# Kernel optimization log

Hardware: AMD Instinct MI355X
Metric: run time of the kernel (lower is better)

The kernel has to match this reference:

```python
import jax, jax.numpy as jnp
import numpy as np

LRU_DIM = 256
HIDDEN = 256
H = 64
N = LRU_DIM // H  # 4 (even, per assert)
R_MIN, R_MAX, MAX_PHASE = 0.9, 0.999, 6.28
BSZ, T = 8, 4096


def _rotate_half(x):
    # interleaved pairs: [x0,x1,x2,x3,...] -> [-x1,x0,-x3,x2,...]
    r = jnp.stack([-x[..., 1::2], x[..., 0::2]], axis=-1)
    return r.reshape(x.shape)


def _mix_sequence(gamma, thetas, Us):
    # gamma: scalar, thetas: (N/2,), Us: (T,B,N) -> (T,B,N)
    Tlen = Us.shape[0]
    gammas = jnp.broadcast_to(gamma, (Tlen,))
    ths = jnp.broadcast_to(thetas, (Tlen,) + thetas.shape)

    def binf(a, b):
        gi, ti, xi = a
        gj, tj, xj = b
        theta = jnp.repeat(tj, 2, axis=-1)            # (T, N): [t0,t0,t1,t1,...]
        sin = jnp.sin(theta)[..., None, :]            # (T,1,N)
        cos = jnp.cos(theta)[..., None, :]
        acc = gj[..., None, None] * (cos * xi + sin * _rotate_half(xi)) + xj
        return (gi * gj, ti + tj, acc)

    _, _, res = jax.lax.associative_scan(binf, (gammas, ths, Us), axis=0)
    return res


def setup_inputs() -> dict:
    key = jax.random.key(0)
    ks = jax.random.split(key, 7)
    scale = 1.0 / np.sqrt(HIDDEN + LRU_DIM)
    u = jax.random.normal(ks[0], (BSZ, HIDDEN, T), dtype=jnp.float32)
    thetas_log = jnp.log(jax.random.uniform(ks[1], (H, N // 2), minval=0.01, maxval=1.0) * MAX_PHASE).astype(jnp.float32)
    P_param = (jax.random.normal(ks[2], (H, N, N), dtype=jnp.float32) / np.sqrt(LRU_DIM + N)).astype(jnp.float32)
    B_param = (jax.random.normal(ks[3], (H, N, HIDDEN), dtype=jnp.float32) * scale).astype(jnp.float32)
    C = (jax.random.normal(ks[4], (HIDDEN, LRU_DIM), dtype=jnp.float32) * scale).astype(jnp.float32)
    D = jax.random.normal(ks[5], (HIDDEN,), dtype=jnp.float32)
    u1 = jax.random.uniform(ks[6], (H,))
    gamma_log = (np.log(-np.log(R_MAX)) + u1 * (np.log(-np.log(R_MIN)) - np.log(-np.log(R_MAX)))).astype(jnp.float32)
    return {"u": u, "thetas_log": thetas_log, "P_param": P_param,
            "B_param": B_param, "C": C, "D": D, "gamma_log": gamma_log}


def reference(u, thetas_log, P_param, B_param, C, D, gamma_log):
    Bsz, hidden, Tlen = u.shape
    ut = jnp.transpose(u, (0, 2, 1))                       # (B,T,Dh)
    gamma = jnp.exp(-jnp.exp(gamma_log))                   # (H,)
    trace_per_head = jnp.sum(B_param * B_param, axis=(1, 2))  # tr(B B^T) per head
    norm = jnp.sqrt((1.0 - gamma ** 2) / trace_per_head)
    B_norm = norm[:, None, None] * B_param                 # (H,N,Dh)
    skew = P_param - jnp.swapaxes(P_param, 1, 2)
    P = jax.vmap(jax.scipy.linalg.expm)(skew)              # (H,N,N), orthogonal
    Us = jnp.einsum('HnD,BTD->HTBn', B_norm, ut)           # (H,T,B,N)
    Us = jnp.einsum('HNn,HTBn->HTBN', P, Us)               # == einsum with P^T as in torch
    thetas = jnp.exp(thetas_log)                           # (H,N/2)
    y = jax.vmap(_mix_sequence)(gamma, thetas, Us)         # (H,T,B,N)
    y = jnp.einsum('HNn,HTBN->HTBn', P, y)
    y = jnp.transpose(y, (2, 1, 0, 3)).reshape(Bsz, Tlen, -1)  # (B,T,lru_dim)
    y = jnp.einsum('Dn,BTn->BTD', C, y) + D * ut
    return jnp.transpose(y, (0, 2, 1))                     # (B,Dh,T)
```

## Files before the change

kernel.cpp:

```cpp
#include <hip/hip_runtime.h>
#include <math.h>


typedef __attribute__((ext_vector_type(8))) short short8;
typedef __attribute__((ext_vector_type(4))) float f32x4;

#define TLEN 4096
#define LCH 32
#define NCH 128
#define BSZ 8
#define LDW 132
#define LDK 264

constexpr int MB_OFF   = 0;
constexpr int CB_OFF   = 32768;
constexpr int AP_OFF   = 65536;
constexpr int ALP_OFF  = AP_OFF + (LCH + 1) * 256;
constexpr int TOT_OFF  = ALP_OFF + (NCH + 1) * 256;
constexpr int ZST_OFF  = TOT_OFF + NCH * BSZ * 256;

__device__ __forceinline__ float bfbits2f(unsigned int bits16) {
  union { unsigned int u; float f; } v; v.u = bits16 << 16; return v.f;
}
__device__ __forceinline__ unsigned int f2bfbits(float f) {
  union { float f; unsigned int u; } v; v.f = f;
  return (v.u + 0x7fffu + ((v.u >> 16) & 1u)) >> 16;
}
__device__ __forceinline__ unsigned int pack2(float x, float y) {
  return f2bfbits(x) | (f2bfbits(y) << 16);
}

__global__ __launch_bounds__(256) void k0_setup(
    const float* __restrict__ thetas_log, const float* __restrict__ P_param,
    const float* __restrict__ B_param, const float* __restrict__ C,
    const float* __restrict__ gamma_log, float* __restrict__ ws) {
  const int h = blockIdx.x;
  const int tid = threadIdx.x;
  __shared__ float red[4];
  __shared__ float Psh[16];
  __shared__ float nrmsh;

  {
    float4 v = *(const float4*)(B_param + (size_t)h * 1024 + tid * 4);
    float s = v.x * v.x + v.y * v.y + v.z * v.z + v.w * v.w;
#pragma unroll
    for (int off = 32; off > 0; off >>= 1) s += __shfl_down(s, off);
    if ((tid & 63) == 0) red[tid >> 6] = s;
  }
  __syncthreads();

  if (tid == 0) {
    double A[4][4], E[4][4], Tm[4][4];
    for (int i = 0; i < 4; ++i)
      for (int j = 0; j < 4; ++j)
        A[i][j] = (double)P_param[h * 16 + i * 4 + j] - (double)P_param[h * 16 + j * 4 + i];
    double fro = 0.0;
    for (int i = 0; i < 4; ++i) for (int j = 0; j < 4; ++j) fro += A[i][j] * A[i][j];
    fro = sqrt(fro);
    int s = 0;
    while (fro > 0.25 && s < 30) { fro *= 0.5; ++s; }
    double scl = 1.0;
    for (int q2 = 0; q2 < s; ++q2) scl *= 0.5;
    for (int i = 0; i < 4; ++i) for (int j = 0; j < 4; ++j) A[i][j] *= scl;
    for (int i = 0; i < 4; ++i)
      for (int j = 0; j < 4; ++j) { E[i][j] = (i == j) ? 1.0 : 0.0; Tm[i][j] = E[i][j]; }
    for (int k = 1; k <= 16; ++k) {
      double Tn[4][4];
      for (int i = 0; i < 4; ++i)
        for (int j = 0; j < 4; ++j) {
          double acc = 0.0;
          for (int m = 0; m < 4; ++m) acc += Tm[i][m] * A[m][j];
          Tn[i][j] = acc / (double)k;
        }
      for (int i = 0; i < 4; ++i)
        for (int j = 0; j < 4; ++j) { Tm[i][j] = Tn[i][j]; E[i][j] += Tn[i][j]; }
    }
    for (int q2 = 0; q2 < s; ++q2) {
      double E2[4][4];
      for (int i = 0; i < 4; ++i)
        for (int j = 0; j < 4; ++j) {
          double acc = 0.0;
          for (int m = 0; m < 4; ++m) acc += E[i][m] * E[m][j];
          E2[i][j] = acc;
        }
      for (int i = 0; i < 4; ++i) for (int j = 0; j < 4; ++j) E[i][j] = E2[i][j];
    }
    for (int i = 0; i < 4; ++i)
      for (int j = 0; j < 4; ++j) Psh[i * 4 + j] = (float)E[i][j];
  } else if (tid == 64 || tid == 65) {
    const int p = h * 2 + (tid - 64);
    double th = exp((double)thetas_log[p]);
    double g = exp(-exp((double)gamma_log[h]));
    double ar = g * cos(th), ai = g * sin(th);
    float2* Apw = (float2*)(ws + AP_OFF);
    double xr = 1.0, xi = 0.0;
    Apw[p] = make_float2(1.f, 0.f);
    for (int j = 1; j <= LCH; ++j) {
      double nr = xr * ar - xi * ai, ni = xr * ai + xi * ar;
      xr = nr; xi = ni;
      Apw[j * 128 + p] = make_float2((float)xr, (float)xi);
    }
  } else if (tid == 128) {
    double g = exp(-exp((double)gamma_log[h]));
    double tr = (double)red[0] + red[1] + red[2] + red[3];
    nrmsh = (float)sqrt((1.0 - g * g) / tr);
  }
  __syncthreads();

  unsigned short* Mbf = (unsigned short*)(ws + MB_OFF);
  unsigned int*   Cbd = (unsigned int*)(ws + CB_OFF);
  {
    float b0 = B_param[(h * 4 + 0) * 256 + tid];
    float b1 = B_param[(h * 4 + 1) * 256 + tid];
    float b2 = B_param[(h * 4 + 2) * 256 + tid];
    float b3 = B_param[(h * 4 + 3) * 256 + tid];
    float nrm = nrmsh;
#pragma unroll
    for (int N = 0; N < 4; ++N) {
      float acc = Psh[N * 4 + 0] * b0 + Psh[N * 4 + 1] * b1 +
                  Psh[N * 4 + 2] * b2 + Psh[N * 4 + 3] * b3;
      Mbf[(h * 4 + N) * 256 + tid] = (unsigned short)f2bfbits(nrm * acc);
    }
  }
  {
    float4 cv = *(const float4*)(C + (size_t)tid * 256 + h * 4);
    float o[4];
#pragma unroll
    for (int N = 0; N < 4; ++N)
      o[N] = cv.x * Psh[N * 4 + 0] + cv.y * Psh[N * 4 + 1] +
             cv.z * Psh[N * 4 + 2] + cv.w * Psh[N * 4 + 3];
    Cbd[(tid * 256 + h * 4) >> 1]       = pack2(o[0], o[1]);
    Cbd[((tid * 256 + h * 4) >> 1) + 1] = pack2(o[2], o[3]);
  }
}

__global__ __launch_bounds__(256, 4) void k1_mfma(
    const float* __restrict__ u, float* __restrict__ ws) {
  __shared__ __align__(16) unsigned short us[LCH * LDK];
  __shared__ __align__(16) unsigned int   wd[LCH * LDW];

  const int c = blockIdx.x, b = blockIdx.y;
  const int t0 = c * LCH;
  const int tid = threadIdx.x;
  const int L = tid & 63;
  const int w = __builtin_amdgcn_readfirstlane(tid >> 6);
  const int qh = L >> 4, l15 = L & 15;

  {
    unsigned int* usd = (unsigned int*)us;
    const int dp = tid >> 3;
    const int t4 = (tid & 7) * 4;
    f32x4 va[4], vb[4];
#pragma unroll
    for (int i = 0; i < 4; ++i) {
      int j = dp + 32 * i;
      va[i] = *(const f32x4*)(u + (size_t)(b * 256 + 2 * j) * TLEN + t0 + t4);
      vb[i] = *(const f32x4*)(u + (size_t)(b * 256 + 2 * j + 1) * TLEN + t0 + t4);
    }
#pragma unroll
    for (int i = 0; i < 4; ++i) {
      int j = dp + 32 * i;
#pragma unroll
      for (int dt = 0; dt < 4; ++dt)
        usd[(t4 + dt) * LDW + j] = pack2(va[i][dt], vb[i][dt]);
    }
  }
  __syncthreads();

  f32x4 acc[4][2];
#pragma unroll
  for (int rt = 0; rt < 4; ++rt)
#pragma unroll
    for (int tt = 0; tt < 2; ++tt) acc[rt][tt] = (f32x4){0.f, 0.f, 0.f, 0.f};
  {
    const unsigned short* Mbf = (const unsigned short*)(ws + MB_OFF);
#pragma unroll
    for (int ks = 0; ks < 8; ++ks) {
      short8 af[4], bf[2];
#pragma unroll
      for (int rt = 0; rt < 4; ++rt)
        af[rt] = *(const short8*)(Mbf + (size_t)(w * 64 + rt * 16 + l15) * 256 + ks * 32 + qh * 8);
#pragma unroll
      for (int tt = 0; tt < 2; ++tt)
        bf[tt] = *(const short8*)(us + (tt * 16 + l15) * LDK + ks * 32 + qh * 8);
#pragma unroll
      for (int rt = 0; rt < 4; ++rt)
#pragma unroll
        for (int tt = 0; tt < 2; ++tt)
          acc[rt][tt] = __builtin_amdgcn_mfma_f32_16x16x32_bf16(af[rt], bf[tt], acc[rt][tt], 0, 0, 0);
    }
  }

#pragma unroll
  for (int rt = 0; rt < 4; ++rt) {
    int pbase = w * 32 + rt * 8 + qh * 2;
#pragma unroll
    for (int tt = 0; tt < 2; ++tt) {
      int t = tt * 16 + l15;
      f32x4 a4 = acc[rt][tt];
      wd[t * LDW + pbase]     = pack2(a4[0], a4[1]);
      wd[t * LDW + pbase + 1] = pack2(a4[2], a4[3]);
    }
  }
  __syncthreads();

  if (tid < 128) {
    const int p = tid;
    const float2* Apw = (const float2*)(ws + AP_OFF);
    unsigned int* Zg = (unsigned int*)(ws + ZST_OFF) + (size_t)(c * BSZ + b) * 4096;
    float2 a = Apw[128 + p];
    float zr = 0.f, zi = 0.f;
#pragma unroll
    for (int t = 0; t < LCH; ++t) {
      unsigned int wv = wd[t * LDW + p];
      float wr = bfbits2f(wv & 0xffffu), wi = bfbits2f(wv >> 16);
      float nr = fmaf(a.x, zr, fmaf(-a.y, zi, wr));
      float ni = fmaf(a.x, zi, fmaf(a.y, zr, wi));
      zr = nr; zi = ni;
      Zg[t * 128 + p] = pack2(zr, zi);
    }
    ((float2*)(ws + TOT_OFF))[(c * BSZ + b) * 128 + p] = make_float2(zr, zi);
  }
}

__global__ __launch_bounds__(128) void k2_carry(float* __restrict__ ws) {
  const int b = blockIdx.x;
  const int p = threadIdx.x;
  const float2* Apw = (const float2*)(ws + AP_OFF);
  float2* Tot = (float2*)(ws + TOT_OFF);
  const float2 aL = Apw[LCH * 128 + p];
  float cr = 0.f, ci = 0.f;
  for (int c0 = 0; c0 < NCH; c0 += 16) {
    float2 tv[16];
#pragma unroll
    for (int k = 0; k < 16; ++k)
      tv[k] = Tot[(size_t)((c0 + k) * BSZ + b) * 128 + p];
#pragma unroll
    for (int k = 0; k < 16; ++k) {
      Tot[(size_t)((c0 + k) * BSZ + b) * 128 + p] = make_float2(cr, ci);
      float nr = fmaf(aL.x, cr, fmaf(-aL.y, ci, tv[k].x));
      float ni = fmaf(aL.x, ci, fmaf(aL.y, cr, tv[k].y));
      cr = nr; ci = ni;
    }
  }
}

__global__ __launch_bounds__(256, 4) void k3_mfma(
    const float* __restrict__ u, const float* __restrict__ Dv,
    const float* __restrict__ ws, float* __restrict__ out) {
  __shared__ __align__(16) unsigned char smem[LCH * LDK * 2];
  unsigned int* wd = (unsigned int*)smem;

  const int c = blockIdx.x, b = blockIdx.y;
  const int t0 = c * LCH;
  const int tid = threadIdx.x;
  const int L = tid & 63;
  const int w = __builtin_amdgcn_readfirstlane(tid >> 6);
  const int qh = L >> 4, l15 = L & 15;

  {
    const int p = tid & 127;
    const float2 cv = ((const float2*)(ws + TOT_OFF))[(size_t)(c * BSZ + b) * 128 + p];
    const float2* Apw = (const float2*)(ws + AP_OFF);
    const unsigned int* Zg = (const unsigned int*)(ws + ZST_OFF) + (size_t)(c * BSZ + b) * 4096;
    unsigned int zv[16];
#pragma unroll
    for (int jj = 0; jj < 16; ++jj)
      zv[jj] = Zg[tid + 256 * jj];
#pragma unroll
    for (int jj = 0; jj < 16; ++jj) {
      int t = (tid + 256 * jj) >> 7;
      float2 ap = Apw[(t + 1) * 128 + p];
      float sr = fmaf(ap.x, cv.x, fmaf(-ap.y, cv.y, bfbits2f(zv[jj] & 0xffffu)));
      float si = fmaf(ap.x, cv.y, fmaf(ap.y, cv.x, bfbits2f(zv[jj] >> 16)));
      wd[t * LDW + p] = pack2(sr, si);
    }
  }
  __syncthreads();

  f32x4 acc[4][2];
#pragma unroll
  for (int rt = 0; rt < 4; ++rt)
#pragma unroll
    for (int tt = 0; tt < 2; ++tt) acc[rt][tt] = (f32x4){0.f, 0.f, 0.f, 0.f};
  {
    const unsigned short* Cbf = (const unsigned short*)(ws + CB_OFF);
    const unsigned short* zs  = (const unsigned short*)smem;
#pragma unroll
    for (int ks = 0; ks < 8; ++ks) {
      short8 af[4], bf[2];
#pragma unroll
      for (int rt = 0; rt < 4; ++rt)
        af[rt] = *(const short8*)(Cbf + (size_t)(w * 64 + rt * 16 + l15) * 256 + ks * 32 + qh * 8);
#pragma unroll
      for (int tt = 0; tt < 2; ++tt)
        bf[tt] = *(const short8*)(zs + (tt * 16 + l15) * LDK + ks * 32 + qh * 8);
#pragma unroll
      for (int rt = 0; rt < 4; ++rt)
#pragma unroll
        for (int tt = 0; tt < 2; ++tt)
          acc[rt][tt] = __builtin_amdgcn_mfma_f32_16x16x32_bf16(af[rt], bf[tt], acc[rt][tt], 0, 0, 0);
    }
  }

  float dv[4][4];
#pragma unroll
  for (int rt = 0; rt < 4; ++rt)
#pragma unroll
    for (int q = 0; q < 4; ++q) dv[rt][q] = Dv[w * 64 + rt * 16 + qh * 4 + q];
#pragma unroll
  for (int rt = 0; rt < 4; ++rt) {
    int Dbase = w * 64 + rt * 16 + qh * 4;
#pragma unroll
    for (int tt = 0; tt < 2; ++tt) {
      int t = tt * 16 + l15;
      f32x4 a4 = acc[rt][tt];
      size_t obase = (size_t)(b * 256 + Dbase) * TLEN + t0 + t;
      float uv[4];
#pragma unroll
      for (int q = 0; q < 4; ++q)
        uv[q] = u[obase + (size_t)q * TLEN];
#pragma unroll
      for (int q = 0; q < 4; ++q)
        out[obase + (size_t)q * TLEN] = a4[q] + dv[rt][q] * uv[q];
    }
  }
}

extern "C" void kernel_launch(void* const* d_in, const int* in_sizes, int n_in,
                              void* d_out, int out_size, void* d_ws, size_t ws_size,
                              hipStream_t stream) {
  const float* u          = (const float*)d_in[0];
  const float* thetas_log = (const float*)d_in[1];
  const float* P_param    = (const float*)d_in[2];
  const float* B_param    = (const float*)d_in[3];
  const float* C          = (const float*)d_in[4];
  const float* Dvec       = (const float*)d_in[5];
  const float* gamma_log  = (const float*)d_in[6];
  float* out = (float*)d_out;
  float* ws  = (float*)d_ws;

  hipLaunchKernelGGL(k0_setup, dim3(64), dim3(256), 0, stream,
                     thetas_log, P_param, B_param, C, gamma_log, ws);
  hipLaunchKernelGGL(k1_mfma, dim3(NCH, BSZ), dim3(256), 0, stream, u, ws);
  hipLaunchKernelGGL(k2_carry, dim3(BSZ), dim3(128), 0, stream, ws);
  hipLaunchKernelGGL(k3_mfma, dim3(NCH, BSZ), dim3(256), 0, stream, u, Dvec, ws, out);
}
```

Before: 156.3 us.

## Fuse local C-projection into chunk scan kernel and add linear carry correction

The chunk-local scan states are no longer written to global memory and re-read. k1 projects them through C in shared memory, adds the D*u skip term using the bf16 u already in shared memory, and writes the output directly. k3 becomes a correction pass that projects only the carry contribution A^t*carry, exploiting linearity, and adds it to out with a read-modify-write. Chunk 0 is skipped because its carry is zero. This removes the large Z staging traffic and the second read of u. In exchange it reads out back from memory, duplicates the MFMA work, and the skip term now uses the bf16-rounded u.

```diff
diff --git a/kernel.cpp b/kernel.cpp
--- a/kernel.cpp
+++ b/kernel.cpp
@@ -17,7 +17,6 @@
 constexpr int AP_OFF   = 65536;
 constexpr int ALP_OFF  = AP_OFF + (LCH + 1) * 256;
 constexpr int TOT_OFF  = ALP_OFF + (NCH + 1) * 256;
-constexpr int ZST_OFF  = TOT_OFF + NCH * BSZ * 256;
 
 __device__ __forceinline__ float bfbits2f(unsigned int bits16) {
   union { unsigned int u; float f; } v; v.u = bits16 << 16; return v.f;
@@ -135,7 +134,8 @@
 }
 
 __global__ __launch_bounds__(256, 4) void k1_mfma(
-    const float* __restrict__ u, float* __restrict__ ws) {
+    const float* __restrict__ u, const float* __restrict__ Dv,
+    float* __restrict__ ws, float* __restrict__ out) {
   __shared__ __align__(16) unsigned short us[LCH * LDK];
   __shared__ __align__(16) unsigned int   wd[LCH * LDW];
 
@@ -207,7 +207,6 @@
   if (tid < 128) {
     const int p = tid;
     const float2* Apw = (const float2*)(ws + AP_OFF);
-    unsigned int* Zg = (unsigned int*)(ws + ZST_OFF) + (size_t)(c * BSZ + b) * 4096;
     float2 a = Apw[128 + p];
     float zr = 0.f, zi = 0.f;
 #pragma unroll
@@ -217,9 +216,58 @@
       float nr = fmaf(a.x, zr, fmaf(-a.y, zi, wr));
       float ni = fmaf(a.x, zi, fmaf(a.y, zr, wi));
       zr = nr; zi = ni;
-      Zg[t * 128 + p] = pack2(zr, zi);
+      wd[t * LDW + p] = pack2(zr, zi);
     }
     ((float2*)(ws + TOT_OFF))[(c * BSZ + b) * 128 + p] = make_float2(zr, zi);
+  }
+  __syncthreads();
+
+  f32x4 acc2[4][2];
+#pragma unroll
+  for (int rt = 0; rt < 4; ++rt)
+#pragma unroll
+    for (int tt = 0; tt < 2; ++tt) acc2[rt][tt] = (f32x4){0.f, 0.f, 0.f, 0.f};
+  {
+    const unsigned short* Cbf = (const unsigned short*)(ws + CB_OFF);
+    const unsigned short* zs  = (const unsigned short*)wd;
+#pragma unroll
+    for (int ks = 0; ks < 8; ++ks) {
+      short8 af[4], bf[2];
+#pragma unroll
+      for (int rt = 0; rt < 4; ++rt)
+        af[rt] = *(const short8*)(Cbf + (size_t)(w * 64 + rt * 16 + l15) * 256 + ks * 32 + qh * 8);
+#pragma unroll
+      for (int tt = 0; tt < 2; ++tt)
+        bf[tt] = *(const short8*)(zs + (tt * 16 + l15) * LDK + ks * 32 + qh * 8);
+#pragma unroll
+      for (int rt = 0; rt < 4; ++rt)
+#pragma unroll
+        for (int tt = 0; tt < 2; ++tt)
+          acc2[rt][tt] = __builtin_amdgcn_mfma_f32_16x16x32_bf16(af[rt], bf[tt], acc2[rt][tt], 0, 0, 0);
+    }
+  }
+
+  float dv[4][4];
+#pragma unroll
+  for (int rt = 0; rt < 4; ++rt)
+#pragma unroll
+    for (int q = 0; q < 4; ++q) dv[rt][q] = Dv[w * 64 + rt * 16 + qh * 4 + q];
+#pragma unroll
+  for (int rt = 0; rt < 4; ++rt) {
+    int Dbase = w * 64 + rt * 16 + qh * 4;
+#pragma unroll
+    for (int tt = 0; tt < 2; ++tt) {
+      int t = tt * 16 + l15;
+      f32x4 a4 = acc2[rt][tt];
+      unsigned int u01 = *(const unsigned int*)(us + t * LDK + Dbase);
+      unsigned int u23 = *(const unsigned int*)(us + t * LDK + Dbase + 2);
+      float uv[4] = {bfbits2f(u01 & 0xffffu), bfbits2f(u01 >> 16),
+                     bfbits2f(u23 & 0xffffu), bfbits2f(u23 >> 16)};
+      size_t obase = (size_t)(b * 256 + Dbase) * TLEN + t0 + t;
+#pragma unroll
+      for (int q = 0; q < 4; ++q)
+        out[obase + (size_t)q * TLEN] = a4[q] + dv[rt][q] * uv[q];
+    }
   }
 }
 
@@ -245,13 +293,11 @@
   }
 }
 
-__global__ __launch_bounds__(256, 4) void k3_mfma(
-    const float* __restrict__ u, const float* __restrict__ Dv,
+__global__ __launch_bounds__(256, 4) void k3_corr(
     const float* __restrict__ ws, float* __restrict__ out) {
-  __shared__ __align__(16) unsigned char smem[LCH * LDK * 2];
-  unsigned int* wd = (unsigned int*)smem;
-
-  const int c = blockIdx.x, b = blockIdx.y;
+  __shared__ __align__(16) unsigned int wd[LCH * LDW];
+
+  const int c = blockIdx.x + 1, b = blockIdx.y;
   const int t0 = c * LCH;
   const int tid = threadIdx.x;
   const int L = tid & 63;
@@ -260,19 +306,15 @@
 
   {
     const int p = tid & 127;
+    const int thalf = (tid >> 7) * 16;
     const float2 cv = ((const float2*)(ws + TOT_OFF))[(size_t)(c * BSZ + b) * 128 + p];
     const float2* Apw = (const float2*)(ws + AP_OFF);
-    const unsigned int* Zg = (const unsigned int*)(ws + ZST_OFF) + (size_t)(c * BSZ + b) * 4096;
-    unsigned int zv[16];
-#pragma unroll
-    for (int jj = 0; jj < 16; ++jj)
-      zv[jj] = Zg[tid + 256 * jj];
-#pragma unroll
-    for (int jj = 0; jj < 16; ++jj) {
-      int t = (tid + 256 * jj) >> 7;
+#pragma unroll
+    for (int tt2 = 0; tt2 < 16; ++tt2) {
+      int t = thalf + tt2;
       float2 ap = Apw[(t + 1) * 128 + p];
-      float sr = fmaf(ap.x, cv.x, fmaf(-ap.y, cv.y, bfbits2f(zv[jj] & 0xffffu)));
-      float si = fmaf(ap.x, cv.y, fmaf(ap.y, cv.x, bfbits2f(zv[jj] >> 16)));
+      float sr = fmaf(ap.x, cv.x, -ap.y * cv.y);
+      float si = fmaf(ap.x, cv.y,  ap.y * cv.x);
       wd[t * LDW + p] = pack2(sr, si);
     }
   }
@@ -285,7 +327,7 @@
     for (int tt = 0; tt < 2; ++tt) acc[rt][tt] = (f32x4){0.f, 0.f, 0.f, 0.f};
   {
     const unsigned short* Cbf = (const unsigned short*)(ws + CB_OFF);
-    const unsigned short* zs  = (const unsigned short*)smem;
+    const unsigned short* zs  = (const unsigned short*)wd;
 #pragma unroll
     for (int ks = 0; ks < 8; ++ks) {
       short8 af[4], bf[2];
@@ -303,11 +345,6 @@
     }
   }
 
-  float dv[4][4];
-#pragma unroll
-  for (int rt = 0; rt < 4; ++rt)
-#pragma unroll
-    for (int q = 0; q < 4; ++q) dv[rt][q] = Dv[w * 64 + rt * 16 + qh * 4 + q];
 #pragma unroll
   for (int rt = 0; rt < 4; ++rt) {
     int Dbase = w * 64 + rt * 16 + qh * 4;
@@ -316,13 +353,13 @@
       int t = tt * 16 + l15;
       f32x4 a4 = acc[rt][tt];
       size_t obase = (size_t)(b * 256 + Dbase) * TLEN + t0 + t;
-      float uv[4];
+      float ov[4];
 #pragma unroll
       for (int q = 0; q < 4; ++q)
-        uv[q] = u[obase + (size_t)q * TLEN];
+        ov[q] = out[obase + (size_t)q * TLEN];
 #pragma unroll
       for (int q = 0; q < 4; ++q)
-        out[obase + (size_t)q * TLEN] = a4[q] + dv[rt][q] * uv[q];
+        out[obase + (size_t)q * TLEN] = ov[q] + a4[q];
     }
   }
 }
@@ -342,7 +379,9 @@
 
   hipLaunchKernelGGL(k0_setup, dim3(64), dim3(256), 0, stream,
                      thetas_log, P_param, B_param, C, gamma_log, ws);
-  hipLaunchKernelGGL(k1_mfma, dim3(NCH, BSZ), dim3(256), 0, stream, u, ws);
+  hipLaunchKernelGGL(k1_mfma, dim3(NCH, BSZ), dim3(256), 0, stream,
+                     u, Dvec, ws, out);
   hipLaunchKernelGGL(k2_carry, dim3(BSZ), dim3(128), 0, stream, ws);
-  hipLaunchKernelGGL(k3_mfma, dim3(NCH, BSZ), dim3(256), 0, stream, u, Dvec, ws, out);
-}
+  hipLaunchKernelGGL(k3_corr, dim3(NCH - 1, BSZ), dim3(256), 0, stream,
+                     ws, out);
+}
```

Measured after the change: 182.9 us. +17.0%, slower.
